# Kernel tuning notes

Measured on AMD Instinct MI355X. Metric: run time of the kernel, lower is better.

## Reference

```python
import jax, jax.numpy as jnp
import numpy as np
from jax.scipy.special import logsumexp

SPARSITY = 0.0


def setup_inputs() -> dict:
    key = jax.random.key(0)
    k1, k2, k3, k4, k5 = jax.random.split(key, 5)
    N, M = 65536, 1024
    sample = jax.random.uniform(k1, (N, 2), dtype=jnp.float32)
    mu = jax.random.uniform(k2, (M, 2), dtype=jnp.float32)
    sigma_log = jax.random.uniform(k3, (M, 2), dtype=jnp.float32)
    theta = jax.random.normal(k4, (M,), dtype=jnp.float32)
    w = jax.random.normal(k5, (M, 1), dtype=jnp.float32)
    return {"sample": sample, "mu": mu, "sigma_log": sigma_log, "theta": theta, "w": w}


def reference(sample, mu, sigma_log, theta, w):
    # Anisotropic covariance entries: gamma_j = R(theta)^T diag(sig2) R(theta)
    sig2 = jnp.exp(-2.0 * sigma_log)            # [M,2], inverse variances
    a, b = sig2[:, 0], sig2[:, 1]
    c, s = jnp.cos(theta), jnp.sin(theta)
    g11 = a * c**2 + b * s**2                   # [M]
    g12 = (a - b) * c * s                       # [M]
    g22 = a * s**2 + b * c**2                   # [M]

    # Log weights: log_softmax(w) - sum(sigma_log) (normalization factor)
    wlog = jax.nn.log_softmax(w, axis=0)[:, 0] - sigma_log.sum(axis=1)  # [M]

    # All-pairs anisotropic quadratic form, fused per-coordinate (no [N,M,2] tensor)
    dx = sample[:, None, 0] - mu[None, :, 0]    # [N,M]
    dy = sample[:, None, 1] - mu[None, :, 1]    # [N,M]
    qf = g11 * dx * dx + 2.0 * g12 * dx * dy + g22 * dy * dy  # [N,M]

    # Log-density at each sample: logsumexp over mixture components
    ll = logsumexp(wlog[None, :] - qf, axis=1)  # [N]

    # Negative log-likelihood + sparsity penalty
    nll = -ll.sum() + SPARSITY * jnp.sqrt(jax.nn.softmax(w, axis=0)).sum()
    return nll
```

## Files before the change

kernel.cpp:

```cpp
#include <hip/hip_runtime.h>
#include <math.h>

#define LOG2E 1.4426950408889634f
#define LN2   0.6931471805599453f

typedef short bf8 __attribute__((ext_vector_type(8)));
typedef float f4  __attribute__((ext_vector_type(4)));

__device__ __forceinline__ unsigned short bf_hi(float x) {
    unsigned u = __float_as_uint(x);
    return (unsigned short)((u + 0x7FFFu + ((u >> 16) & 1u)) >> 16);
}

__global__ __launch_bounds__(1024) void gm_single(
    const float* __restrict__ sample,
    const float* __restrict__ mu,
    const float* __restrict__ sigma_log,
    const float* __restrict__ theta,
    const float* __restrict__ w,
    float* __restrict__ acc,
    unsigned* __restrict__ cnt,
    float* __restrict__ out)
{
    __shared__ __align__(16) unsigned short wrec[1024 * 40];
    __shared__ __align__(16) unsigned short srec[256 * 40];
    __shared__ float ws[16];
    __shared__ float psum[16 * 256];
    __shared__ float bsum[4];

    const int tid  = threadIdx.x;
    const int lane = tid & 63;
    const int wid  = tid >> 6;
    const int quad = lane >> 4;
    const int col  = lane & 15;

    const float wj = w[tid];
    float e = __expf(wj);
    #pragma unroll
    for (int off = 32; off > 0; off >>= 1)
        e += __shfl_down(e, off, 64);
    if (lane == 0) ws[wid] = e;
    __syncthreads();
    float tot = 0.0f;
    #pragma unroll
    for (int k = 0; k < 16; ++k) tot += ws[k];
    const float lse = __logf(tot);

    {
        const float sl0 = sigma_log[2 * tid + 0];
        const float sl1 = sigma_log[2 * tid + 1];
        const float a = __expf(-2.0f * sl0);
        const float b = __expf(-2.0f * sl1);
        const float th = theta[tid];
        const float c = __cosf(th);
        const float s = __sinf(th);

        const float g11 = a * c * c + b * s * s;
        const float g12 = (a - b) * c * s;
        const float g22 = a * s * s + b * c * c;
        const float mx = mu[2 * tid + 0];
        const float my = mu[2 * tid + 1];
        const float wlog = wj - lse - (sl0 + sl1);

        float cf[6];
        cf[0] = -g11 * LOG2E;
        cf[1] = -2.0f * g12 * LOG2E;
        cf[2] = -g22 * LOG2E;
        cf[3] = 2.0f * (g11 * mx + g12 * my) * LOG2E;
        cf[4] = 2.0f * (g12 * mx + g22 * my) * LOG2E;
        const float F = g11 * mx * mx + 2.0f * g12 * mx * my + g22 * my * my;
        cf[5] = (wlog - F) * LOG2E;

        unsigned short r[32];
        #pragma unroll
        for (int q = 0; q < 6; ++q) {
            const unsigned short h = bf_hi(cf[q]);
            const float hf = __uint_as_float((unsigned)h << 16);
            const unsigned short l = bf_hi(cf[q] - hf);
            r[q] = h; r[6 + q] = l; r[12 + q] = h;
        }
        #pragma unroll
        for (int q = 18; q < 32; ++q) r[q] = 0;
        unsigned* dst = (unsigned*)&wrec[tid * 40];
        #pragma unroll
        for (int k = 0; k < 16; ++k)
            dst[k] = ((unsigned)r[2 * k + 1] << 16) | r[2 * k];
    }

    if (tid < 256) {
        const float2 sv = ((const float2*)sample)[blockIdx.x * 256 + tid];
        float f[6];
        f[0] = sv.x * sv.x; f[1] = sv.x * sv.y; f[2] = sv.y * sv.y;
        f[3] = sv.x; f[4] = sv.y; f[5] = 1.0f;
        unsigned short r[32];
        #pragma unroll
        for (int q = 0; q < 6; ++q) {
            const unsigned short h = bf_hi(f[q]);
            const float hf = __uint_as_float((unsigned)h << 16);
            const unsigned short l = bf_hi(f[q] - hf);
            r[q] = h; r[6 + q] = h; r[12 + q] = l;
        }
        #pragma unroll
        for (int q = 18; q < 32; ++q) r[q] = 0;
        unsigned* dst = (unsigned*)&srec[tid * 40];
        #pragma unroll
        for (int k = 0; k < 16; ++k)
            dst[k] = ((unsigned)r[2 * k + 1] << 16) | r[2 * k];
    }
    __syncthreads();

    bf8 afrag[4];
    #pragma unroll
    for (int ct = 0; ct < 4; ++ct)
        afrag[ct] = *(const bf8*)&wrec[(wid * 64 + ct * 16 + col) * 40 + quad * 8];

    const f4 zero = {0.0f, 0.0f, 0.0f, 0.0f};
    for (int st = 0; st < 16; ++st) {
        const bf8 bfrag = *(const bf8*)&srec[(st * 16 + col) * 40 + quad * 8];
        float acc3 = 0.0f;
        #pragma unroll
        for (int ct = 0; ct < 4; ++ct) {
            const f4 d = __builtin_amdgcn_mfma_f32_16x16x32_bf16(
                afrag[ct], bfrag, zero, 0, 0, 0);
            acc3 += (__builtin_amdgcn_exp2f(d[0]) + __builtin_amdgcn_exp2f(d[1]))
                  + (__builtin_amdgcn_exp2f(d[2]) + __builtin_amdgcn_exp2f(d[3]));
        }
        acc3 += __shfl_xor(acc3, 16, 64);
        acc3 += __shfl_xor(acc3, 32, 64);
        if (quad == 0) psum[wid * 256 + st * 16 + col] = acc3;
    }
    __syncthreads();

    if (tid < 256) {
        float t = 0.0f;
        #pragma unroll
        for (int k = 0; k < 16; ++k) t += psum[k * 256 + tid];
        float v = -LN2 * __builtin_amdgcn_logf(t);
        #pragma unroll
        for (int off = 32; off > 0; off >>= 1)
            v += __shfl_down(v, off, 64);
        if ((tid & 63) == 0) bsum[tid >> 6] = v;
    }
    __syncthreads();
    if (tid == 0) {
        const float partial = (bsum[0] + bsum[1]) + (bsum[2] + bsum[3]);
        atomicAdd(acc, partial);
        __threadfence();
        const unsigned old = atomicAdd(cnt, 1u);
        if (old == 0xAAAAAAAAu + 255u) {
            out[0] = atomicAdd(acc, 0.0f);
        }
    }
}

extern "C" void kernel_launch(void* const* d_in, const int* in_sizes, int n_in,
                              void* d_out, int out_size, void* d_ws, size_t ws_size,
                              hipStream_t stream) {
    const float* sample    = (const float*)d_in[0];
    const float* mu        = (const float*)d_in[1];
    const float* sigma_log = (const float*)d_in[2];
    const float* theta     = (const float*)d_in[3];
    const float* w         = (const float*)d_in[4];
    float* out = (float*)d_out;
    float*    acc = (float*)d_ws;
    unsigned* cnt = (unsigned*)((char*)d_ws + 256);

    const int N = in_sizes[0] / 2;

    const int grid = N / 256;
    gm_single<<<grid, 1024, 0, stream>>>(sample, mu, sigma_log, theta, w,
                                         acc, cnt, out);
}
```

Measured before the change: 75.81 us.

## Split LDS records into quad-major planes and drop cross-quad shuffles

The per-row 40-short LDS records are replaced by four quad-major planes of 8 shorts each, padded to 1025/257 rows. Records are written with 16-byte vector stores and fragments are read contiguously, which is meant to cut LDS bank conflicts and store count. The two cross-lane shuffles per step are removed: each quad writes its partial sum into a larger 64-row psum buffer, and the final reduction sums 64 rows with four accumulators. The inner loop is also unrolled by 4. The cost is more LDS (psum grows about fourfold), which may reduce occupancy, plus a longer final reduction.

```diff
diff --git a/kernel.cpp b/kernel.cpp
--- a/kernel.cpp
+++ b/kernel.cpp
@@ -22,10 +22,10 @@
     unsigned* __restrict__ cnt,
     float* __restrict__ out)
 {
-    __shared__ __align__(16) unsigned short wrec[1024 * 40];
-    __shared__ __align__(16) unsigned short srec[256 * 40];
+    __shared__ __align__(16) unsigned short wrecq[4][1025][8];
+    __shared__ __align__(16) unsigned short srecq[4][257][8];
     __shared__ float ws[16];
-    __shared__ float psum[16 * 256];
+    __shared__ float psum[64][260];
     __shared__ float bsum[4];
 
     const int tid  = threadIdx.x;
@@ -81,10 +81,15 @@
         }
         #pragma unroll
         for (int q = 18; q < 32; ++q) r[q] = 0;
-        unsigned* dst = (unsigned*)&wrec[tid * 40];
         #pragma unroll
-        for (int k = 0; k < 16; ++k)
-            dst[k] = ((unsigned)r[2 * k + 1] << 16) | r[2 * k];
+        for (int q = 0; q < 4; ++q) {
+            uint4 v;
+            v.x = ((unsigned)r[q * 8 + 1] << 16) | r[q * 8 + 0];
+            v.y = ((unsigned)r[q * 8 + 3] << 16) | r[q * 8 + 2];
+            v.z = ((unsigned)r[q * 8 + 5] << 16) | r[q * 8 + 4];
+            v.w = ((unsigned)r[q * 8 + 7] << 16) | r[q * 8 + 6];
+            *reinterpret_cast<uint4*>(&wrecq[q][tid][0]) = v;
+        }
     }
 
     if (tid < 256) {
@@ -102,21 +107,28 @@
         }
         #pragma unroll
         for (int q = 18; q < 32; ++q) r[q] = 0;
-        unsigned* dst = (unsigned*)&srec[tid * 40];
         #pragma unroll
-        for (int k = 0; k < 16; ++k)
-            dst[k] = ((unsigned)r[2 * k + 1] << 16) | r[2 * k];
+        for (int q = 0; q < 4; ++q) {
+            uint4 v;
+            v.x = ((unsigned)r[q * 8 + 1] << 16) | r[q * 8 + 0];
+            v.y = ((unsigned)r[q * 8 + 3] << 16) | r[q * 8 + 2];
+            v.z = ((unsigned)r[q * 8 + 5] << 16) | r[q * 8 + 4];
+            v.w = ((unsigned)r[q * 8 + 7] << 16) | r[q * 8 + 6];
+            *reinterpret_cast<uint4*>(&srecq[q][tid][0]) = v;
+        }
     }
     __syncthreads();
 
     bf8 afrag[4];
     #pragma unroll
     for (int ct = 0; ct < 4; ++ct)
-        afrag[ct] = *(const bf8*)&wrec[(wid * 64 + ct * 16 + col) * 40 + quad * 8];
+        afrag[ct] = *(const bf8*)&wrecq[quad][wid * 64 + ct * 16 + col][0];
 
     const f4 zero = {0.0f, 0.0f, 0.0f, 0.0f};
+    float* prow = &psum[wid * 4 + quad][0];
+    #pragma unroll 4
     for (int st = 0; st < 16; ++st) {
-        const bf8 bfrag = *(const bf8*)&srec[(st * 16 + col) * 40 + quad * 8];
+        const bf8 bfrag = *(const bf8*)&srecq[quad][st * 16 + col][0];
         float acc3 = 0.0f;
         #pragma unroll
         for (int ct = 0; ct < 4; ++ct) {
@@ -125,17 +137,20 @@
             acc3 += (__builtin_amdgcn_exp2f(d[0]) + __builtin_amdgcn_exp2f(d[1]))
                   + (__builtin_amdgcn_exp2f(d[2]) + __builtin_amdgcn_exp2f(d[3]));
         }
-        acc3 += __shfl_xor(acc3, 16, 64);
-        acc3 += __shfl_xor(acc3, 32, 64);
-        if (quad == 0) psum[wid * 256 + st * 16 + col] = acc3;
+        prow[st * 16 + col] = acc3;
     }
     __syncthreads();
 
     if (tid < 256) {
-        float t = 0.0f;
+        float t0 = 0.f, t1 = 0.f, t2 = 0.f, t3 = 0.f;
         #pragma unroll
-        for (int k = 0; k < 16; ++k) t += psum[k * 256 + tid];
-        float v = -LN2 * __builtin_amdgcn_logf(t);
+        for (int k = 0; k < 64; k += 4) {
+            t0 += psum[k + 0][tid];
+            t1 += psum[k + 1][tid];
+            t2 += psum[k + 2][tid];
+            t3 += psum[k + 3][tid];
+        }
+        float v = -LN2 * __builtin_amdgcn_logf((t0 + t1) + (t2 + t3));
         #pragma unroll
         for (int off = 32; off > 0; off >>= 1)
             v += __shfl_down(v, off, 64);
```

Measured after the change: 75.76 us. No clear change (-0.1%).
